# Performance work log

Hardware: AMD Instinct MI355X
Metric: run time of the kernel (lower is better)

The kernel has to match this reference:

```python
import jax, jax.numpy as jnp
import numpy as np

EPS = 1e-6       # eps from __init__
STEPSIZE = 1.0   # stepsize from __init__
DELTA = 0.1      # delta from __init__


def setup_inputs() -> dict:
    key = jax.random.key(0)
    k1, k2, k3 = jax.random.split(key, 3)
    N, L, H, E, M = 2, 2048, 8, 64, 64
    return {
        "queries": jax.random.normal(k1, (N, L, H, E), dtype=jnp.float32),
        "keys": jax.random.normal(k2, (N, L, H, E), dtype=jnp.float32),
        "values": jax.random.normal(k3, (N, L, H, M), dtype=jnp.float32),
        "key_lengths_mask": jnp.ones((N, L), dtype=jnp.float32),
    }


def reference(queries, keys, values, key_lengths_mask):
    # elu feature map: elu(x) + 1
    Q = jax.nn.elu(queries) + 1.0                                   # [N,L,H,E]
    K = (jax.nn.elu(keys) + 1.0) * key_lengths_mask[:, :, None, None]
    N, L, H, E = Q.shape

    # normalizer Z_t = 1 / (q_t . sum_{s<=t} k_s + eps)
    Z = 1.0 / (jnp.einsum('nlhe,nlhe->nlh', Q, jnp.cumsum(K, axis=1)) + EPS)

    # per-step outer products k_s v_s^T  (original materializes this einsum)
    KV = jnp.einsum('nlhe,nlhm->nlhem', K, values)                  # [N,L,H,E,M]

    # causal_dot_product: out_t = q_t . cumsum_s(KV)_t
    out = jnp.einsum('nlhe,nlhem->nlhm', Q, jnp.cumsum(KV, axis=1)) * Z[..., None]

    # momentum coefficients mu_j from Frobenius norms over (E,M)
    diff_norm = jnp.sqrt(jnp.sum((KV[:, 1:] - KV[:, :-1]) ** 2, axis=(3, 4)))  # [N,L-1,H]
    base_norm = jnp.sqrt(jnp.sum(KV[:, :-1] ** 2, axis=(3, 4)))
    mu = jnp.clip((1.0 - jnp.sqrt(diff_norm / base_norm)) ** 2, 0.0, 1.0 - DELTA)

    # momentum weights: a_{L-1}=1, a_j = 1 + mu_j * a_{j+1} (backward recurrence).
    # This equals both momentum_weight (cumprod-sum form) and momentum_weight_old
    # (explicit reverse loop) in the original, so Kn == Kw.
    def step(a, mu_t):
        a_new = 1.0 + mu_t * a
        return a_new, a_new

    _, a_seq = jax.lax.scan(step, jnp.ones((N, H), Q.dtype),
                            jnp.moveaxis(mu, 1, 0), reverse=True)   # [L-1,N,H]
    momentum_weight = jnp.concatenate(
        [jnp.moveaxis(a_seq, 0, 1), jnp.ones((N, 1, H), Q.dtype)], axis=1)  # [N,L,H]
    Kn = K * momentum_weight[..., None] * STEPSIZE                  # [N,L,H,E]

    return out, Kn
```

## Files before the change

kernel.cpp:

```cpp
#include <hip/hip_runtime.h>

#define N_ 2
#define L_ 2048
#define H_ 8
#define NH_ 16
#define NC_ 32
#define EPS_ 1e-6f
#define DELTA_ 0.1f

#define CHSZ 4160
#define ST_SHORTS (NH_*NC_*CHSZ)
#define KV_SHORTS (NH_*L_*64)

typedef short s8v __attribute__((ext_vector_type(8)));
typedef short s4v __attribute__((ext_vector_type(4)));
typedef float f4v __attribute__((ext_vector_type(4)));

__device__ __forceinline__ float elup1(float x){ return x>0.f ? x+1.f : __expf(x); }
__device__ __forceinline__ short f2b(float x){
  unsigned u = __float_as_uint(x);
  return (short)((u + 0x7FFFu + ((u>>16)&1u)) >> 16);
}
__device__ __forceinline__ float b2f(short s){
  return __uint_as_float(((unsigned)(unsigned short)s) << 16);
}

__global__ __launch_bounds__(256) void kA(const float* __restrict__ keys,
    const float* __restrict__ values, const float* __restrict__ mask,
    unsigned short* __restrict__ st, short* __restrict__ ktil,
    short* __restrict__ vtil, float* __restrict__ mu)
{
  const int bid = blockIdx.x, c = bid & (NC_-1), nh = bid >> 5;
  const int n = nh >> 3, h = nh & 7, tid = threadIdx.x;
  const int lane = tid & 63, w = tid >> 6, r = lane & 15, g = lane >> 4;

  __shared__ __attribute__((aligned(16))) short Ktb[64][72];
  __shared__ __attribute__((aligned(16))) short Vtb[80][72];
  __shared__ float prt[6][4][64];

  #pragma unroll
  for (int i = 0; i < 4; ++i) {
    const int idx4 = tid + 256*i;
    const int t = idx4 >> 4, e4 = (idx4 & 15) << 2;
    const int l = c*64 + t;
    const size_t b = (((size_t)n*L_ + l)*H_ + h)*64 + e4;
    const float m0 = mask[n*L_ + l];
    const f4v kx = *(const f4v*)&keys[b];
    const f4v vx = *(const f4v*)&values[b];
    s4v kb4, vb4;
    #pragma unroll
    for (int j = 0; j < 4; ++j) {
      kb4[j] = f2b(elup1(kx[j]) * m0);
      vb4[j] = f2b(vx[j]);
    }
    *(s4v*)&ktil[((size_t)nh*L_ + l)*64 + e4] = kb4;
    *(s4v*)&vtil[((size_t)nh*L_ + l)*64 + e4] = vb4;
    #pragma unroll
    for (int j = 0; j < 4; ++j) { Ktb[e4+j][t] = kb4[j]; Vtb[e4+j][t] = vb4[j]; }
  }
  if (tid < 64) Vtb[64][tid] = (short)0x3F80;
  __syncthreads();

  {
    f4v acc[5];
    #pragma unroll
    for (int j = 0; j < 5; ++j) acc[j] = (f4v)(0.f);
    #pragma unroll
    for (int k2 = 0; k2 < 2; ++k2) {
      const s8v a = *(const s8v*)&Ktb[w*16 + r][k2*32 + g*8];
      #pragma unroll
      for (int mj = 0; mj < 5; ++mj) {
        const s8v bb = *(const s8v*)&Vtb[mj*16 + r][k2*32 + g*8];
        acc[mj] = __builtin_amdgcn_mfma_f32_16x16x32_bf16(a, bb, acc[mj], 0, 0, 0);
      }
    }
    unsigned short* sp = st + (size_t)bid*CHSZ;
    #pragma unroll
    for (int mj = 0; mj < 5; ++mj) {
      const int m = mj*16 + r;
      if (m <= 64) {
        s4v pk;
        #pragma unroll
        for (int j = 0; j < 4; ++j) pk[j] = f2b(acc[mj][j]);
        *(s4v*)&sp[(size_t)m*64 + w*16 + g*4] = pk;
      }
    }
  }

  {
    const int t = lane, eq = w;
    const int l = c*64 + t;
    const int l1 = (l+1 < L_) ? l+1 : l;
    const size_t b0 = (((size_t)n*L_ + l )*H_ + h)*64 + eq*16;
    const size_t b1 = (((size_t)n*L_ + l1)*H_ + h)*64 + eq*16;
    const float m0 = mask[n*L_ + l], m1 = mask[n*L_ + l1];
    float kk0=0.f,kk1=0.f,knn=0.f,vv0=0.f,vv1=0.f,vnn=0.f;
    #pragma unroll
    for (int j = 0; j < 16; j += 4) {
      const f4v ka = *(const f4v*)&keys[b0+j];
      const f4v kc = *(const f4v*)&keys[b1+j];
      const f4v va = *(const f4v*)&values[b0+j];
      const f4v vc = *(const f4v*)&values[b1+j];
      #pragma unroll
      for (int jj = 0; jj < 4; ++jj) {
        const float k0 = elup1(ka[jj])*m0, k1 = elup1(kc[jj])*m1;
        kk0 += k0*k0; kk1 += k1*k1; knn += k0*k1;
        const float v0 = va[jj], v1 = vc[jj];
        vv0 += v0*v0; vv1 += v1*v1; vnn += v0*v1;
      }
    }
    prt[0][eq][t]=kk0; prt[1][eq][t]=kk1; prt[2][eq][t]=knn;
    prt[3][eq][t]=vv0; prt[4][eq][t]=vv1; prt[5][eq][t]=vnn;
  }
  __syncthreads();
  if (tid < 64) {
    float s[6];
    #pragma unroll
    for (int q2 = 0; q2 < 6; ++q2)
      s[q2] = prt[q2][0][tid]+prt[q2][1][tid]+prt[q2][2][tid]+prt[q2][3][tid];
    const int j = c*64 + tid;
    float mval = 0.f;
    if (j < L_-1) {
      const float base2 = s[0]*s[3];
      float diff2 = s[1]*s[4] - 2.f*s[2]*s[5] + base2;
      diff2 = fmaxf(diff2, 0.f);
      if (base2 > 0.f) {
        const float r4 = sqrtf(sqrtf(diff2/base2));
        const float om = 1.f - r4;
        mval = fminf(om*om, 1.f - DELTA_);
      } else {
        mval = 1.f - DELTA_;
      }
    }
    mu[(size_t)nh*L_ + j] = mval;
  }
}

__global__ __launch_bounds__(256) void kBC(unsigned short* __restrict__ st,
    const float* __restrict__ mu, float* __restrict__ aw)
{
  const int bx = blockIdx.x, tid = threadIdx.x;
  if (bx < 260) {
    const int id = bx*256 + tid;
    const int nh2 = id / CHSZ;
    const int elem = id - nh2*CHSZ;
    unsigned short* base = st + (size_t)nh2*NC_*CHSZ + elem;
    unsigned short rr[NC_];
    #pragma unroll
    for (int c2 = 0; c2 < NC_; ++c2) rr[c2] = base[(size_t)c2*CHSZ];
    float acc = 0.f;
    #pragma unroll
    for (int c2 = 0; c2 < NC_; ++c2) {
      const float v = b2f((short)rr[c2]);
      base[(size_t)c2*CHSZ] = (unsigned short)f2b(acc);
      acc += v;
    }
    return;
  }
  const int nh2 = bx - 260;
  const float* mup = mu + (size_t)nh2*L_;
  float* awp = aw + (size_t)nh2*L_;
  __shared__ float Psc[256], Qsc[256];
  float lm[8];
  #pragma unroll
  for (int i = 0; i < 8; ++i) lm[i] = mup[tid*8 + i];
  float p = 1.f, q = 0.f;
  #pragma unroll
  for (int i = 7; i >= 0; --i) { q = lm[i]*q + 1.f; p *= lm[i]; }
  Psc[tid] = p; Qsc[tid] = q;
  __syncthreads();
  for (int d = 1; d < 256; d <<= 1) {
    float pr = 1.f, qr = 0.f;
    const bool has = (tid + d) < 256;
    if (has) { pr = Psc[tid+d]; qr = Qsc[tid+d]; }
    __syncthreads();
    if (has) { const float np = p*pr, nq = p*qr + q; p = np; q = nq; Psc[tid] = p; Qsc[tid] = q; }
    __syncthreads();
  }
  float x = (tid == 255) ? 1.f : Psc[tid+1] + Qsc[tid+1];
  #pragma unroll
  for (int i = 7; i >= 0; --i) { x = lm[i]*x + 1.f; awp[tid*8+i] = x; }
}

__global__ __launch_bounds__(256) void kD(const float* __restrict__ queries,
    const unsigned short* __restrict__ st, const short* __restrict__ ktil,
    const short* __restrict__ vtil, const float* __restrict__ aw,
    float* __restrict__ out, float* __restrict__ kn)
{
  const int bid = blockIdx.x, c = bid & (NC_-1), nh = bid >> 5;
  const int n = nh >> 3, h = nh & 7, tid = threadIdx.x;
  const int lane = tid & 63, w = tid >> 6, r = lane & 15, g = lane >> 4;

  __shared__ __attribute__((aligned(16))) short Qb[64][72];
  __shared__ __attribute__((aligned(16))) short Kb[64][72];
  __shared__ __attribute__((aligned(16))) short Vtb[80][72];
  __shared__ __attribute__((aligned(16))) union {
    struct { short Pb[64][72]; short Sb[80][72]; } d;
    float outf[64][68];
  } U;
  __shared__ float Zl[64], al[64];

  #pragma unroll
  for (int i = 0; i < 4; ++i) {
    const int idx4 = tid + 256*i;
    const int t = idx4 >> 4, e4 = (idx4 & 15) << 2;
    const int l = c*64 + t;
    const f4v qx = *(const f4v*)&queries[(((size_t)n*L_ + l)*H_ + h)*64 + e4];
    s4v qb4;
    #pragma unroll
    for (int j = 0; j < 4; ++j) qb4[j] = f2b(elup1(qx[j]));
    *(s4v*)&Qb[t][e4] = qb4;
  }
  for (int idx = tid; idx < 512; idx += 256) {
    const int t = idx >> 3, e8 = (idx & 7) << 3;
    *(s8v*)&Kb[t][e8] = *(const s8v*)&ktil[((size_t)nh*L_ + c*64 + t)*64 + e8];
  }
  #pragma unroll
  for (int i = 0; i < 4; ++i) {
    const int idx4 = tid + 256*i;
    const int t = idx4 >> 4, m4 = (idx4 & 15) << 2;
    const s4v vb4 = *(const s4v*)&vtil[((size_t)nh*L_ + c*64 + t)*64 + m4];
    #pragma unroll
    for (int j = 0; j < 4; ++j) Vtb[m4+j][t] = vb4[j];
  }
  for (int idx = tid; idx < 16*72; idx += 256) {
    const int rr = idx/72, cc = idx - rr*72;
    Vtb[64+rr][cc] = (rr==0 && cc<64) ? (short)0x3F80 : (short)0;
  }
  {
    const unsigned short* sp = st + (size_t)bid*CHSZ;
    for (int idx = tid; idx < 520; idx += 256) {
      const int m = idx >> 3, e8 = (idx & 7) << 3;
      *(s8v*)&U.d.Sb[m][e8] = *(const s8v*)&sp[(size_t)m*64 + e8];
    }
    for (int idx = 520 + tid; idx < 640; idx += 256) {
      const int m = idx >> 3, e8 = (idx & 7) << 3;
      *(s8v*)&U.d.Sb[m][e8] = (s8v)(0);
    }
  }
  if (tid < 64) al[tid] = aw[(size_t)nh*L_ + c*64 + tid];
  __syncthreads();

  {
    f4v pacc[4];
    #pragma unroll
    for (int tj = 0; tj < 4; ++tj) pacc[tj] = (f4v)(0.f);
    #pragma unroll
    for (int k2 = 0; k2 < 2; ++k2) {
      const s8v a = *(const s8v*)&Kb[w*16 + r][k2*32 + g*8];
      #pragma unroll
      for (int tj = 0; tj < 4; ++tj) {
        const s8v bb = *(const s8v*)&Qb[tj*16 + r][k2*32 + g*8];
        pacc[tj] = __builtin_amdgcn_mfma_f32_16x16x32_bf16(a, bb, pacc[tj], 0, 0, 0);
      }
    }
    #pragma unroll
    for (int tj = 0; tj < 4; ++tj) {
      const int t = tj*16 + r;
      s4v pk;
      #pragma unroll
      for (int j = 0; j < 4; ++j) {
        const int s2 = w*16 + g*4 + j;
        pk[j] = (s2 <= t) ? f2b(pacc[tj][j]) : (short)0;
      }
      *(s4v*)&U.d.Pb[t][w*16 + g*4] = pk;
    }
  }
  __syncthreads();

  f4v oacc[5];
  #pragma unroll
  for (int j = 0; j < 5; ++j) oacc[j] = (f4v)(0.f);
  #pragma unroll
  for (int k2 = 0; k2 < 4; ++k2) {
    const s8v a = (k2 < 2) ? *(const s8v*)&Qb[w*16 + r][k2*32 + g*8]
                           : *(const s8v*)&U.d.Pb[w*16 + r][(k2-2)*32 + g*8];
    #pragma unroll
    for (int mj = 0; mj < 5; ++mj) {
      const s8v bb = (k2 < 2) ? *(const s8v*)&U.d.Sb[mj*16 + r][k2*32 + g*8]
                              : *(const s8v*)&Vtb[mj*16 + r][(k2-2)*32 + g*8];
      oacc[mj] = __builtin_amdgcn_mfma_f32_16x16x32_bf16(a, bb, oacc[mj], 0, 0, 0);
    }
  }
  __syncthreads();

  if (r == 0) {
    #pragma unroll
    for (int j = 0; j < 4; ++j) Zl[w*16 + g*4 + j] = 1.f / (oacc[4][j] + EPS_);
  }
  #pragma unroll
  for (int mj = 0; mj < 4; ++mj)
    #pragma unroll
    for (int j = 0; j < 4; ++j)
      U.outf[w*16 + g*4 + j][mj*16 + r] = oacc[mj][j];
  __syncthreads();

  for (int idx = tid; idx < 1024; idx += 256) {
    const int t = idx >> 4, m4 = (idx & 15) << 2, l = c*64 + t;
    f4v v = *(const f4v*)&U.outf[t][m4];
    const float z = Zl[t];
    v[0] *= z; v[1] *= z; v[2] *= z; v[3] *= z;
    *(f4v*)&out[(((size_t)n*L_ + l)*H_ + h)*64 + m4] = v;
  }
  for (int idx = tid; idx < 1024; idx += 256) {
    const int t = idx >> 4, e4 = (idx & 15) << 2, l = c*64 + t;
    const float a2 = al[t];
    const s4v kb4 = *(const s4v*)&Kb[t][e4];
    f4v o;
    #pragma unroll
    for (int j = 0; j < 4; ++j) o[j] = b2f(kb4[j]) * a2;
    *(f4v*)&kn[(((size_t)n*L_ + l)*H_ + h)*64 + e4] = o;
  }
}

extern "C" void kernel_launch(void* const* d_in, const int* in_sizes, int n_in,
                              void* d_out, int out_size, void* d_ws, size_t ws_size,
                              hipStream_t stream) {
  (void)in_sizes; (void)n_in; (void)out_size; (void)ws_size;
  const float* queries = (const float*)d_in[0];
  const float* keys    = (const float*)d_in[1];
  const float* values  = (const float*)d_in[2];
  const float* mask    = (const float*)d_in[3];
  float* out = (float*)d_out;
  float* kn  = out + (size_t)N_*L_*H_*64;

  unsigned short* st = (unsigned short*)d_ws;
  short* ktil = (short*)(st + ST_SHORTS);
  short* vtil = ktil + KV_SHORTS;
  float* mu = (float*)(vtil + KV_SHORTS);
  float* aw = mu + NH_*L_;

  hipLaunchKernelGGL(kA,  dim3(NH_*NC_), dim3(256), 0, stream,
                     keys, values, mask, st, ktil, vtil, mu);
  hipLaunchKernelGGL(kBC, dim3(276),     dim3(256), 0, stream, st, mu, aw);
  hipLaunchKernelGGL(kD,  dim3(NH_*NC_), dim3(256), 0, stream,
                     queries, st, ktil, vtil, aw, out, kn);
}
```

Before: 29.90 us.

## Fold chunk-state prefix sum and momentum scan into the output kernel

Removes the middle kBC kernel. Each kD block now sums the bf16 chunk states of all earlier chunks itself, and every block redundantly runs the 256-wide backward scan of mu to obtain its own 64 momentum weights. This drops one launch and one global round trip. In exchange, later chunks do up to 31 redundant state reads and every block repeats the scan. The added 2 KB of shared memory may also lower occupancy.

```diff
diff --git a/kernel.cpp b/kernel.cpp
--- a/kernel.cpp
+++ b/kernel.cpp
@@ -136,55 +136,9 @@
   }
 }
 
-__global__ __launch_bounds__(256) void kBC(unsigned short* __restrict__ st,
-    const float* __restrict__ mu, float* __restrict__ aw)
-{
-  const int bx = blockIdx.x, tid = threadIdx.x;
-  if (bx < 260) {
-    const int id = bx*256 + tid;
-    const int nh2 = id / CHSZ;
-    const int elem = id - nh2*CHSZ;
-    unsigned short* base = st + (size_t)nh2*NC_*CHSZ + elem;
-    unsigned short rr[NC_];
-    #pragma unroll
-    for (int c2 = 0; c2 < NC_; ++c2) rr[c2] = base[(size_t)c2*CHSZ];
-    float acc = 0.f;
-    #pragma unroll
-    for (int c2 = 0; c2 < NC_; ++c2) {
-      const float v = b2f((short)rr[c2]);
-      base[(size_t)c2*CHSZ] = (unsigned short)f2b(acc);
-      acc += v;
-    }
-    return;
-  }
-  const int nh2 = bx - 260;
-  const float* mup = mu + (size_t)nh2*L_;
-  float* awp = aw + (size_t)nh2*L_;
-  __shared__ float Psc[256], Qsc[256];
-  float lm[8];
-  #pragma unroll
-  for (int i = 0; i < 8; ++i) lm[i] = mup[tid*8 + i];
-  float p = 1.f, q = 0.f;
-  #pragma unroll
-  for (int i = 7; i >= 0; --i) { q = lm[i]*q + 1.f; p *= lm[i]; }
-  Psc[tid] = p; Qsc[tid] = q;
-  __syncthreads();
-  for (int d = 1; d < 256; d <<= 1) {
-    float pr = 1.f, qr = 0.f;
-    const bool has = (tid + d) < 256;
-    if (has) { pr = Psc[tid+d]; qr = Qsc[tid+d]; }
-    __syncthreads();
-    if (has) { const float np = p*pr, nq = p*qr + q; p = np; q = nq; Psc[tid] = p; Qsc[tid] = q; }
-    __syncthreads();
-  }
-  float x = (tid == 255) ? 1.f : Psc[tid+1] + Qsc[tid+1];
-  #pragma unroll
-  for (int i = 7; i >= 0; --i) { x = lm[i]*x + 1.f; awp[tid*8+i] = x; }
-}
-
 __global__ __launch_bounds__(256) void kD(const float* __restrict__ queries,
     const unsigned short* __restrict__ st, const short* __restrict__ ktil,
-    const short* __restrict__ vtil, const float* __restrict__ aw,
+    const short* __restrict__ vtil, const float* __restrict__ mu,
     float* __restrict__ out, float* __restrict__ kn)
 {
   const int bid = blockIdx.x, c = bid & (NC_-1), nh = bid >> 5;
@@ -198,6 +152,7 @@
     struct { short Pb[64][72]; short Sb[80][72]; } d;
     float outf[64][68];
   } U;
+  __shared__ float Psc[256], Qsc[256];
   __shared__ float Zl[64], al[64];
 
   #pragma unroll
@@ -227,18 +182,73 @@
     const int rr = idx/72, cc = idx - rr*72;
     Vtb[64+rr][cc] = (rr==0 && cc<64) ? (short)0x3F80 : (short)0;
   }
-  {
-    const unsigned short* sp = st + (size_t)bid*CHSZ;
-    for (int idx = tid; idx < 520; idx += 256) {
-      const int m = idx >> 3, e8 = (idx & 7) << 3;
-      *(s8v*)&U.d.Sb[m][e8] = *(const s8v*)&sp[(size_t)m*64 + e8];
+
+  {
+    float a0[8], a1[8], a2[8];
+    #pragma unroll
+    for (int j = 0; j < 8; ++j) { a0[j] = 0.f; a1[j] = 0.f; a2[j] = 0.f; }
+    const unsigned short* basep = st + (size_t)nh*NC_*CHSZ;
+    for (int ch = 0; ch < c; ++ch) {
+      const unsigned short* sp = basep + (size_t)ch*CHSZ;
+      const s8v v0 = *(const s8v*)&sp[(size_t)tid*8];
+      const s8v v1 = *(const s8v*)&sp[(size_t)(tid+256)*8];
+      #pragma unroll
+      for (int j = 0; j < 8; ++j) {
+        a0[j] += b2f((short)v0[j]);
+        a1[j] += b2f((short)v1[j]);
+      }
+      if (tid < 8) {
+        const s8v v2 = *(const s8v*)&sp[(size_t)(tid+512)*8];
+        #pragma unroll
+        for (int j = 0; j < 8; ++j) a2[j] += b2f((short)v2[j]);
+      }
+    }
+    {
+      s8v o0, o1;
+      #pragma unroll
+      for (int j = 0; j < 8; ++j) { o0[j] = f2b(a0[j]); o1[j] = f2b(a1[j]); }
+      *(s8v*)&U.d.Sb[tid>>3][(tid&7)<<3] = o0;
+      const int gi = tid + 256;
+      *(s8v*)&U.d.Sb[gi>>3][(gi&7)<<3] = o1;
+      if (tid < 8) {
+        s8v o2;
+        #pragma unroll
+        for (int j = 0; j < 8; ++j) o2[j] = f2b(a2[j]);
+        *(s8v*)&U.d.Sb[64][tid<<3] = o2;
+      }
     }
     for (int idx = 520 + tid; idx < 640; idx += 256) {
-      const int m = idx >> 3, e8 = (idx & 7) << 3;
-      *(s8v*)&U.d.Sb[m][e8] = (s8v)(0);
-    }
-  }
-  if (tid < 64) al[tid] = aw[(size_t)nh*L_ + c*64 + tid];
+      *(s8v*)&U.d.Sb[idx>>3][(idx&7)<<3] = (s8v)(0);
+    }
+  }
+
+  {
+    const float* mup = mu + (size_t)nh*L_;
+    float lm[8];
+    const f4v m0 = *(const f4v*)&mup[tid*8];
+    const f4v m1 = *(const f4v*)&mup[tid*8+4];
+    #pragma unroll
+    for (int j = 0; j < 4; ++j) { lm[j] = m0[j]; lm[4+j] = m1[j]; }
+    float p = 1.f, q = 0.f;
+    #pragma unroll
+    for (int i = 7; i >= 0; --i) { q = lm[i]*q + 1.f; p *= lm[i]; }
+    Psc[tid] = p; Qsc[tid] = q;
+    __syncthreads();
+    for (int d = 1; d < 256; d <<= 1) {
+      float pr = 1.f, qr = 0.f;
+      const bool has = (tid + d) < 256;
+      if (has) { pr = Psc[tid+d]; qr = Qsc[tid+d]; }
+      __syncthreads();
+      if (has) { const float np = p*pr, nq = p*qr + q; p = np; q = nq; Psc[tid] = p; Qsc[tid] = q; }
+      __syncthreads();
+    }
+    if ((tid >> 3) == c) {
+      float x = (tid == 255) ? 1.f : Psc[tid+1] + Qsc[tid+1];
+      const int d0 = (tid & 7) << 3;
+      #pragma unroll
+      for (int i = 7; i >= 0; --i) { x = lm[i]*x + 1.f; al[d0 + i] = x; }
+    }
+  }
   __syncthreads();
 
   {
@@ -328,11 +338,9 @@
   short* ktil = (short*)(st + ST_SHORTS);
   short* vtil = ktil + KV_SHORTS;
   float* mu = (float*)(vtil + KV_SHORTS);
-  float* aw = mu + NH_*L_;
-
-  hipLaunchKernelGGL(kA,  dim3(NH_*NC_), dim3(256), 0, stream,
+
+  hipLaunchKernelGGL(kA, dim3(NH_*NC_), dim3(256), 0, stream,
                      keys, values, mask, st, ktil, vtil, mu);
-  hipLaunchKernelGGL(kBC, dim3(276),     dim3(256), 0, stream, st, mu, aw);
-  hipLaunchKernelGGL(kD,  dim3(NH_*NC_), dim3(256), 0, stream,
-                     queries, st, ktil, vtil, aw, out, kn);
-}
+  hipLaunchKernelGGL(kD, dim3(NH_*NC_), dim3(256), 0, stream,
+                     queries, st, ktil, vtil, mu, out, kn);
+}
```

Result: slower. 38.44 us (+28.6%).
